# Kernel tuning notes

Measured on AMD Instinct MI355X. Metric: run time of the kernel, lower is better.

The kernel has to match this reference:

```python
import jax, jax.numpy as jnp
import numpy as np

DIM = 512
HEADS = 8
D_HEAD = 64
INNER_FF = 4 * DIM  # 2048
EPS = 1e-5
SCALE = D_HEAD ** -0.5


def _layernorm(x, w, b):
    x = x.astype(jnp.float32)
    mu = jnp.mean(x, axis=-1, keepdims=True)
    var = jnp.mean(jnp.square(x - mu), axis=-1, keepdims=True)
    return (x - mu) * jax.lax.rsqrt(var + EPS) * w + b


def _l2_attn(x, wq, bq, wv, bv, wo, bo):
    # x: [B, N, DIM]. k = q (context is ignored in the original module).
    b, n, _ = x.shape
    q = (x @ wq + bq).reshape(b, n, HEADS, D_HEAD).transpose(0, 2, 1, 3)  # b h n d
    v = (x @ wv + bv).reshape(b, n, HEADS, D_HEAD).transpose(0, 2, 1, 3)
    q = q.astype(jnp.float32)
    AB = jnp.einsum('bhid,bhjd->bhij', q, q)          # [b,h,n,n]
    AA = jnp.sum(jnp.square(q), axis=-1)               # [b,h,n]
    sim = -(AA[..., :, None] - 2.0 * AB + AA[..., None, :]) * SCALE
    attn = jax.nn.softmax(sim, axis=-1)
    out = jnp.einsum('bhij,bhjd->bhid', attn, v)       # [b,h,n,d]
    out = out.transpose(0, 2, 1, 3).reshape(b, n, HEADS * D_HEAD)
    return out @ wo + bo


def _geglu_ff(x, w1, b1, w2, b2):
    h = x @ w1 + b1                      # [B, N, 2*INNER_FF]
    a, gate = jnp.split(h, 2, axis=-1)
    return (a * jax.nn.gelu(gate, approximate=False)) @ w2 + b2


def setup_inputs() -> dict:
    key = jax.random.key(0)
    ks = jax.random.split(key, 24)
    s = 0.02
    d = {'x': jax.random.normal(ks[0], (4, 2048, DIM), jnp.float32)}
    # layernorms
    d['sa_norm_w'] = jnp.ones((DIM,), jnp.float32)
    d['sa_norm_b'] = jnp.zeros((DIM,), jnp.float32)
    d['ca_norm_w'] = jnp.ones((DIM,), jnp.float32)
    d['ca_norm_b'] = jnp.zeros((DIM,), jnp.float32)
    d['ff_norm_w'] = jnp.ones((DIM,), jnp.float32)
    d['ff_norm_b'] = jnp.zeros((DIM,), jnp.float32)
    # attn1 (self)
    d['a1_wq'] = jax.random.normal(ks[1], (DIM, DIM), jnp.float32) * s
    d['a1_bq'] = jnp.zeros((DIM,), jnp.float32)
    d['a1_wv'] = jax.random.normal(ks[2], (DIM, DIM), jnp.float32) * s
    d['a1_bv'] = jnp.zeros((DIM,), jnp.float32)
    d['a1_wo'] = jax.random.normal(ks[3], (DIM, DIM), jnp.float32) * s
    d['a1_bo'] = jnp.zeros((DIM,), jnp.float32)
    # attn2 (cross, but k=q and v from x in original code)
    d['a2_wq'] = jax.random.normal(ks[4], (DIM, DIM), jnp.float32) * s
    d['a2_bq'] = jnp.zeros((DIM,), jnp.float32)
    d['a2_wv'] = jax.random.normal(ks[5], (DIM, DIM), jnp.float32) * s
    d['a2_bv'] = jnp.zeros((DIM,), jnp.float32)
    d['a2_wo'] = jax.random.normal(ks[6], (DIM, DIM), jnp.float32) * s
    d['a2_bo'] = jnp.zeros((DIM,), jnp.float32)
    # GEGLU FFN
    d['ff_w1'] = jax.random.normal(ks[7], (DIM, 2 * INNER_FF), jnp.float32) * s
    d['ff_b1'] = jnp.zeros((2 * INNER_FF,), jnp.float32)
    d['ff_w2'] = jax.random.normal(ks[8], (INNER_FF, DIM), jnp.float32) * s
    d['ff_b2'] = jnp.zeros((DIM,), jnp.float32)
    return d


def reference(x, sa_norm_w, sa_norm_b, ca_norm_w, ca_norm_b, ff_norm_w, ff_norm_b,
              a1_wq, a1_bq, a1_wv, a1_bv, a1_wo, a1_bo,
              a2_wq, a2_bq, a2_wv, a2_bv, a2_wo, a2_bo,
              ff_w1, ff_b1, ff_w2, ff_b2):
    x = _l2_attn(_layernorm(x, sa_norm_w, sa_norm_b), a1_wq, a1_bq, a1_wv, a1_bv, a1_wo, a1_bo) + x
    x = _l2_attn(_layernorm(x, ca_norm_w, ca_norm_b), a2_wq, a2_bq, a2_wv, a2_bv, a2_wo, a2_bo) + x
    x = _geglu_ff(_layernorm(x, ff_norm_w, ff_norm_b), ff_w1, ff_b1, ff_w2, ff_b2) + x
    return x
```

## Files before the change

kernel.cpp:

```cpp
#include <hip/hip_runtime.h>
#include <hip/hip_bf16.h>


typedef short bf16x8 __attribute__((ext_vector_type(8)));
typedef float f32x4 __attribute__((ext_vector_type(4)));
typedef unsigned short u16;
typedef unsigned int u32;

__device__ __forceinline__ float bf2f(u16 u) {
    return __uint_as_float(((u32)u) << 16);
}
__device__ __forceinline__ u16 f2bf(float f) {
    u32 u = __float_as_uint(f);
    u32 rb = ((u >> 16) & 1u) + 0x7fffu;
    return (u16)((u + rb) >> 16);
}
__device__ __forceinline__ float gelu_fast(float x) {
    float y = 1.5957691216f * (x + 0.044715f * x * x * x);
    return x / (1.f + __expf(-y));
}
__device__ __forceinline__ void gl2lds16(const u16* g, u16* l) {
    __builtin_amdgcn_global_load_lds(
        (const __attribute__((address_space(1))) void*)(unsigned long long)(uintptr_t)g,
        (__attribute__((address_space(3))) void*)(unsigned long long)(uintptr_t)l,
        16, 0, 0);
}

struct TArgs {
    const float* src[8];
    u16* dst[8];
    int R[8], C[8];
    int start[9];
};
__global__ __launch_bounds__(256) void transpose_multi(TArgs a) {
    __shared__ float tile[32][33];
    int bid = blockIdx.x;
    int s = 0;
    while (bid >= a.start[s + 1]) s++;
    int local = bid - a.start[s];
    int R = a.R[s], C = a.C[s];
    int tx = C >> 5;
    int bx = local % tx, by = local / tx;
    const float* in = a.src[s];
    u16* out = a.dst[s];
    int t = threadIdx.x;
    int c = t & 31, r0 = (t >> 5) * 4;
#pragma unroll
    for (int i = 0; i < 4; i++)
        tile[r0 + i][c] = in[(size_t)(by * 32 + r0 + i) * C + bx * 32 + c];
    __syncthreads();
#pragma unroll
    for (int i = 0; i < 4; i++)
        out[(size_t)(bx * 32 + r0 + i) * R + by * 32 + c] = f2bf(tile[c][r0 + i]);
}

__global__ __launch_bounds__(256) void ln_kernel(const float* __restrict__ x,
                                                 const float* __restrict__ w,
                                                 const float* __restrict__ b,
                                                 u16* __restrict__ out) {
    int row = blockIdx.x, t = threadIdx.x;
    const float* xr = x + (size_t)row * 512;
    float2 v = *(const float2*)(xr + t * 2);
    float s1 = v.x + v.y;
    float s2 = v.x * v.x + v.y * v.y;
#pragma unroll
    for (int m = 1; m < 64; m <<= 1) {
        s1 += __shfl_xor(s1, m);
        s2 += __shfl_xor(s2, m);
    }
    __shared__ float r1[4], r2[4];
    int wave = t >> 6, lane = t & 63;
    if (lane == 0) { r1[wave] = s1; r2[wave] = s2; }
    __syncthreads();
    float tot1 = r1[0] + r1[1] + r1[2] + r1[3];
    float tot2 = r2[0] + r2[1] + r2[2] + r2[3];
    float mu = tot1 * (1.f / 512.f);
    float var = tot2 * (1.f / 512.f) - mu * mu;
    float rs = rsqrtf(var + 1e-5f);
    float2 wv = *(const float2*)(w + t * 2);
    float2 bv = *(const float2*)(b + t * 2);
    float o0 = (v.x - mu) * rs * wv.x + bv.x;
    float o1 = (v.y - mu) * rs * wv.y + bv.y;
    u32 pack = (u32)f2bf(o0) | ((u32)f2bf(o1) << 16);
    *(u32*)(out + (size_t)row * 512 + t * 2) = pack;
}

__global__ __launch_bounds__(256) void gemm_ff1(const u16* __restrict__ A,
                                                const u16* __restrict__ BT,
                                                const float* __restrict__ bias,
                                                u16* __restrict__ gout,
                                                int K) {
    __shared__ u16 As[2][128 * 32];
    __shared__ u16 Bs[2][128 * 32];
    int t = threadIdx.x;
    int wave = t >> 6, lane = t & 63, quad = lane >> 4, l16 = lane & 15;
    int m0 = blockIdx.x * 128, n0 = blockIdx.y * 64;
    f32x4 aacc[2][4], gacc[2][4];
#pragma unroll
    for (int i = 0; i < 2; i++)
#pragma unroll
        for (int j = 0; j < 4; j++) {
            aacc[i][j] = (f32x4){0.f, 0.f, 0.f, 0.f};
            gacc[i][j] = (f32x4){0.f, 0.f, 0.f, 0.f};
        }
    const u16* Ag = A + (size_t)(m0 + wave * 32 + (lane >> 2)) * K + (lane & 3) * 8;
    int brow = (wave < 2) ? (n0 + wave * 32) : (2048 + n0 + (wave - 2) * 32);
    const u16* Bg = BT + (size_t)(brow + (lane >> 2)) * K + (lane & 3) * 8;
    int lo = wave * 32 * 32;
    const size_t rstep = (size_t)16 * K;
    gl2lds16(Ag, &As[0][lo]);
    gl2lds16(Ag + rstep, &As[0][lo + 16 * 32]);
    gl2lds16(Bg, &Bs[0][lo]);
    gl2lds16(Bg + rstep, &Bs[0][lo + 16 * 32]);
    int buf = 0;
    for (int k0 = 0; k0 < K; k0 += 32, buf ^= 1) {
        int kn = (k0 + 32 < K) ? (k0 + 32) : k0;
        int nb = buf ^ 1;
        asm volatile("s_waitcnt lgkmcnt(0)\n\ts_barrier" ::: "memory");
        gl2lds16(Ag + kn, &As[nb][lo]);
        gl2lds16(Ag + kn + rstep, &As[nb][lo + 16 * 32]);
        gl2lds16(Bg + kn, &Bs[nb][lo]);
        gl2lds16(Bg + kn + rstep, &Bs[nb][lo + 16 * 32]);
        asm volatile("s_waitcnt vmcnt(4)\n\ts_barrier" ::: "memory");
        bf16x8 a[2];
#pragma unroll
        for (int i = 0; i < 2; i++)
            a[i] = *(const bf16x8*)&As[buf][(wave * 32 + i * 16 + l16) * 32 + quad * 8];
#pragma unroll
        for (int j = 0; j < 4; j++) {
            bf16x8 ba = *(const bf16x8*)&Bs[buf][(j * 16 + l16) * 32 + quad * 8];
            bf16x8 bg = *(const bf16x8*)&Bs[buf][(64 + j * 16 + l16) * 32 + quad * 8];
#pragma unroll
            for (int i = 0; i < 2; i++) {
                aacc[i][j] = __builtin_amdgcn_mfma_f32_16x16x32_bf16(a[i], ba, aacc[i][j], 0, 0, 0);
                gacc[i][j] = __builtin_amdgcn_mfma_f32_16x16x32_bf16(a[i], bg, gacc[i][j], 0, 0, 0);
            }
        }
    }
    asm volatile("s_waitcnt vmcnt(0)" ::: "memory");
    int row_base = m0 + wave * 32 + quad * 4;
#pragma unroll
    for (int j = 0; j < 4; j++) {
        int col = n0 + j * 16 + l16;
        float ba = bias[col];
        float bg = bias[2048 + col];
#pragma unroll
        for (int i = 0; i < 2; i++) {
#pragma unroll
            for (int r = 0; r < 4; r++) {
                int row = row_base + i * 16 + r;
                float av = aacc[i][j][r] + ba;
                float gv = gacc[i][j][r] + bg;
                gout[(size_t)row * 2048 + col] = f2bf(av * gelu_fast(gv));
            }
        }
    }
}

template <int MODE>
__global__ __launch_bounds__(256) void gemm_rect(const u16* __restrict__ A,
                                                 const u16* __restrict__ BT,
                                                 const float* __restrict__ bias,
                                                 const float* __restrict__ bias2,
                                                 const float* __restrict__ res,
                                                 float* __restrict__ outf,
                                                 u16* __restrict__ outb,
                                                 u16* __restrict__ outb2,
                                                 float* __restrict__ aa,
                                                 int M, int N, int K) {
    __shared__ u16 As[2][128 * 32];
    __shared__ u16 Bs[2][64 * 32];
    int t = threadIdx.x;
    int wave = t >> 6, lane = t & 63, quad = lane >> 4, l16 = lane & 15;
    int m0 = blockIdx.x * 128, n0 = blockIdx.y * 64;
    f32x4 acc[2][4];
#pragma unroll
    for (int i = 0; i < 2; i++)
#pragma unroll
        for (int j = 0; j < 4; j++) acc[i][j] = (f32x4){0.f, 0.f, 0.f, 0.f};
    const u16* Ag = A + (size_t)(m0 + wave * 32 + (lane >> 2)) * K + (lane & 3) * 8;
    const u16* Bg = BT + (size_t)(n0 + wave * 16 + (lane >> 2)) * K + (lane & 3) * 8;
    int loA = wave * 32 * 32;
    int loB = wave * 16 * 32;
    const size_t rstep = (size_t)16 * K;
    gl2lds16(Ag, &As[0][loA]);
    gl2lds16(Ag + rstep, &As[0][loA + 16 * 32]);
    gl2lds16(Bg, &Bs[0][loB]);
    int buf = 0;
    for (int k0 = 0; k0 < K; k0 += 32, buf ^= 1) {
        int kn = (k0 + 32 < K) ? (k0 + 32) : k0;
        int nb = buf ^ 1;
        asm volatile("s_waitcnt lgkmcnt(0)\n\ts_barrier" ::: "memory");
        gl2lds16(Ag + kn, &As[nb][loA]);
        gl2lds16(Ag + kn + rstep, &As[nb][loA + 16 * 32]);
        gl2lds16(Bg + kn, &Bs[nb][loB]);
        asm volatile("s_waitcnt vmcnt(3)\n\ts_barrier" ::: "memory");
        bf16x8 a[2], b[4];
#pragma unroll
        for (int i = 0; i < 2; i++)
            a[i] = *(const bf16x8*)&As[buf][(wave * 32 + i * 16 + l16) * 32 + quad * 8];
#pragma unroll
        for (int j = 0; j < 4; j++)
            b[j] = *(const bf16x8*)&Bs[buf][(j * 16 + l16) * 32 + quad * 8];
#pragma unroll
        for (int i = 0; i < 2; i++)
#pragma unroll
            for (int j = 0; j < 4; j++)
                acc[i][j] = __builtin_amdgcn_mfma_f32_16x16x32_bf16(a[i], b[j], acc[i][j], 0, 0, 0);
    }
    asm volatile("s_waitcnt vmcnt(0)" ::: "memory");
    int row_base = m0 + wave * 32 + quad * 4;
    float ssq[2][4];
#pragma unroll
    for (int i = 0; i < 2; i++)
#pragma unroll
        for (int r = 0; r < 4; r++) ssq[i][r] = 0.f;
#pragma unroll
    for (int j = 0; j < 4; j++) {
        int col = n0 + j * 16 + l16;
        float bv;
        if (MODE == 4) bv = (col < 512) ? bias[col] : bias2[col - 512];
        else bv = bias[col];
#pragma unroll
        for (int i = 0; i < 2; i++) {
            int rowA = row_base + i * 16;
            if (MODE == 4) {
                if (col < 512) {
                    int hh = col >> 6, d = col & 63;
#pragma unroll
                    for (int r = 0; r < 4; r++) {
                        int row = rowA + r;
                        float v = acc[i][j][r] + bv;
                        ssq[i][r] += v * v;
                        outb[((size_t)((row >> 11) * 8 + hh) * 2048 + (row & 2047)) * 64 + d] = f2bf(v);
                    }
                } else {
                    int c2 = col - 512;
                    int hh = c2 >> 6, d = c2 & 63;
                    int n = rowA & 2047;
                    int a4 = (n >> 2) & 7;
                    int ncol = (n & ~31) + ((a4 & 3) << 3) + ((a4 >> 2) << 2);
                    u32 plo = (u32)f2bf(acc[i][j][0] + bv) | ((u32)f2bf(acc[i][j][1] + bv) << 16);
                    u32 phi = (u32)f2bf(acc[i][j][2] + bv) | ((u32)f2bf(acc[i][j][3] + bv) << 16);
                    uint2 pk; pk.x = plo; pk.y = phi;
                    *(uint2*)&outb2[((size_t)((rowA >> 11) * 8 + hh) * 64 + d) * 2048 + ncol] = pk;
                }
            } else {
#pragma unroll
                for (int r = 0; r < 4; r++) {
                    size_t idx = (size_t)(rowA + r) * N + col;
                    outf[idx] = acc[i][j][r] + bv + res[idx];
                }
            }
        }
    }
    if (MODE == 4 && n0 < 512) {
        int hh = n0 >> 6;
#pragma unroll
        for (int i = 0; i < 2; i++) {
#pragma unroll
            for (int r = 0; r < 4; r++) {
                float s = ssq[i][r];
                s += __shfl_xor(s, 1); s += __shfl_xor(s, 2);
                s += __shfl_xor(s, 4); s += __shfl_xor(s, 8);
                if (l16 == 0) {
                    int row = row_base + i * 16 + r;
                    aa[(size_t)((row >> 11) * 8 + hh) * 2048 + (row & 2047)] = s * 0.125f;
                }
            }
        }
    }
}

__global__ __launch_bounds__(256) void attn_mfma(const u16* __restrict__ qbuf,
                                                 const u16* __restrict__ vtp,
                                                 const float* __restrict__ aas,
                                                 u16* __restrict__ out) {
    __shared__ u16 L[2][8192];
    int bid = blockIdx.x;
    int bh = bid & 31;
    int itile = bid >> 5;
    const u16* qb = qbuf + (size_t)bh * 2048 * 64;
    const u16* vtb = vtp + (size_t)bh * 64 * 2048;
    const float* aab = aas + (size_t)bh * 2048;
    int t = threadIdx.x;
    int wave = t >> 6, lane = t & 63, quad = lane >> 4, l16 = lane & 15;
    int ibase = itile * 128 + wave * 32;
    int sw = l16 & 7;

    bf16x8 qf[2][2];
    float ci[2];
    f32x4 O[2][4];
    float lr[2] = {0.f, 0.f};
#pragma unroll
    for (int st = 0; st < 2; st++) {
        const u16* qr = qb + (size_t)(ibase + st * 16 + l16) * 64;
        qf[st][0] = *(const bf16x8*)(qr + quad * 8);
        qf[st][1] = *(const bf16x8*)(qr + 32 + quad * 8);
        ci[st] = aab[ibase + st * 16 + l16];
#pragma unroll
        for (int nt = 0; nt < 4; nt++) O[st][nt] = (f32x4){0.f, 0.f, 0.f, 0.f};
    }

    int r1 = t >> 3, cs = t & 7;
    int wof1 = r1 * 64 + 8 * (cs ^ (r1 & 7));
    int wof2 = (r1 + 32) * 64 + 8 * (cs ^ (r1 & 7));

    {
        uint4 pq1 = *(const uint4*)(qb + (size_t)r1 * 64 + cs * 8);
        uint4 pq2 = *(const uint4*)(qb + (size_t)(r1 + 32) * 64 + cs * 8);
        uint4 pv1 = *(const uint4*)(vtb + (size_t)r1 * 2048 + cs * 8);
        uint4 pv2 = *(const uint4*)(vtb + (size_t)(r1 + 32) * 2048 + cs * 8);
        *(uint4*)&L[0][wof1] = pq1;
        *(uint4*)&L[0][wof2] = pq2;
        *(uint4*)&L[0][4096 + wof1] = pv1;
        *(uint4*)&L[0][4096 + wof2] = pv2;
    }
    __syncthreads();

    for (int it = 0; it < 32; ++it) {
        int cur = it & 1;
        int j0 = it << 6;
        uint4 pq1, pq2, pv1, pv2;
        bool more = (it + 1 < 32);
        if (more) {
            int j0n = j0 + 64;
            pq1 = *(const uint4*)(qb + (size_t)(j0n + r1) * 64 + cs * 8);
            pq2 = *(const uint4*)(qb + (size_t)(j0n + r1 + 32) * 64 + cs * 8);
            pv1 = *(const uint4*)(vtb + (size_t)r1 * 2048 + j0n + cs * 8);
            pv2 = *(const uint4*)(vtb + (size_t)(r1 + 32) * 2048 + j0n + cs * 8);
        }
        const u16* Q = &L[cur][0];
        const u16* V = &L[cur][4096];
#pragma unroll
        for (int c = 0; c < 2; c++) {
            int r10 = c * 32 + l16, r20 = c * 32 + 16 + l16;
            bf16x8 a10 = *(const bf16x8*)&Q[r10 * 64 + 8 * (quad ^ sw)];
            bf16x8 a11 = *(const bf16x8*)&Q[r10 * 64 + 8 * ((4 + quad) ^ sw)];
            bf16x8 a20 = *(const bf16x8*)&Q[r20 * 64 + 8 * (quad ^ sw)];
            bf16x8 a21 = *(const bf16x8*)&Q[r20 * 64 + 8 * ((4 + quad) ^ sw)];
            f32x4 s0[2], s1[2];
            __builtin_amdgcn_s_setprio(1);
#pragma unroll
            for (int st = 0; st < 2; st++) {
                f32x4 z = {0.f, 0.f, 0.f, 0.f};
                s0[st] = __builtin_amdgcn_mfma_f32_16x16x32_bf16(a10, qf[st][0], z, 0, 0, 0);
                s0[st] = __builtin_amdgcn_mfma_f32_16x16x32_bf16(a11, qf[st][1], s0[st], 0, 0, 0);
                s1[st] = __builtin_amdgcn_mfma_f32_16x16x32_bf16(a20, qf[st][0], z, 0, 0, 0);
                s1[st] = __builtin_amdgcn_mfma_f32_16x16x32_bf16(a21, qf[st][1], s1[st], 0, 0, 0);
            }
            __builtin_amdgcn_s_setprio(0);
            float4 aav0 = *(const float4*)(aab + j0 + c * 32 + quad * 4);
            float4 aav1 = *(const float4*)(aab + j0 + c * 32 + 16 + quad * 4);
            bf16x8 pa[2];
#pragma unroll
            for (int st = 0; st < 2; st++) {
                float p0 = __expf(s0[st][0] * 0.25f - aav0.x - ci[st]);
                float p1 = __expf(s0[st][1] * 0.25f - aav0.y - ci[st]);
                float p2 = __expf(s0[st][2] * 0.25f - aav0.z - ci[st]);
                float p3 = __expf(s0[st][3] * 0.25f - aav0.w - ci[st]);
                float p4 = __expf(s1[st][0] * 0.25f - aav1.x - ci[st]);
                float p5 = __expf(s1[st][1] * 0.25f - aav1.y - ci[st]);
                float p6 = __expf(s1[st][2] * 0.25f - aav1.z - ci[st]);
                float p7 = __expf(s1[st][3] * 0.25f - aav1.w - ci[st]);
                lr[st] += (p0 + p1 + p2 + p3) + (p4 + p5 + p6 + p7);
                u32* pu = (u32*)&pa[st];
                pu[0] = __builtin_amdgcn_perm(__float_as_uint(p1), __float_as_uint(p0), 0x07060302u);
                pu[1] = __builtin_amdgcn_perm(__float_as_uint(p3), __float_as_uint(p2), 0x07060302u);
                pu[2] = __builtin_amdgcn_perm(__float_as_uint(p5), __float_as_uint(p4), 0x07060302u);
                pu[3] = __builtin_amdgcn_perm(__float_as_uint(p7), __float_as_uint(p6), 0x07060302u);
            }
            __builtin_amdgcn_s_setprio(1);
#pragma unroll
            for (int nt = 0; nt < 4; nt++) {
                int rv = nt * 16 + l16;
                bf16x8 vf = *(const bf16x8*)&V[rv * 64 + 8 * ((c * 4 + quad) ^ sw)];
                O[0][nt] = __builtin_amdgcn_mfma_f32_16x16x32_bf16(pa[0], vf, O[0][nt], 0, 0, 0);
                O[1][nt] = __builtin_amdgcn_mfma_f32_16x16x32_bf16(pa[1], vf, O[1][nt], 0, 0, 0);
            }
            __builtin_amdgcn_s_setprio(0);
        }
        if (more) {
            u16* D = &L[cur ^ 1][0];
            *(uint4*)&D[wof1] = pq1;
            *(uint4*)&D[wof2] = pq2;
            *(uint4*)&D[4096 + wof1] = pv1;
            *(uint4*)&D[4096 + wof2] = pv2;
        }
        __syncthreads();
    }

    int b = bh >> 3, h = bh & 7;
#pragma unroll
    for (int st = 0; st < 2; st++) {
        float l = lr[st];
        l += __shfl_xor(l, 16);
        l += __shfl_xor(l, 32);
        float inv = 1.f / l;
#pragma unroll
        for (int r = 0; r < 4; r++) {
            float invr = __shfl(inv, quad * 4 + r);
            size_t row = (size_t)(b * 2048 + ibase + st * 16 + quad * 4 + r);
            u16* o = out + row * 512 + h * 64 + l16;
            o[0]  = f2bf(O[st][0][r] * invr);
            o[16] = f2bf(O[st][1][r] * invr);
            o[32] = f2bf(O[st][2][r] * invr);
            o[48] = f2bf(O[st][3][r] * invr);
        }
    }
}

extern "C" void kernel_launch(void* const* d_in, const int* in_sizes, int n_in,
                              void* d_out, int out_size, void* d_ws, size_t ws_size,
                              hipStream_t stream) {
    const float* x      = (const float*)d_in[0];
    const float* sa_w   = (const float*)d_in[1];
    const float* sa_b   = (const float*)d_in[2];
    const float* ca_w   = (const float*)d_in[3];
    const float* ca_b   = (const float*)d_in[4];
    const float* ffn_w  = (const float*)d_in[5];
    const float* ffn_b  = (const float*)d_in[6];
    const float* a1_wq  = (const float*)d_in[7];
    const float* a1_bq  = (const float*)d_in[8];
    const float* a1_wv  = (const float*)d_in[9];
    const float* a1_bv  = (const float*)d_in[10];
    const float* a1_wo  = (const float*)d_in[11];
    const float* a1_bo  = (const float*)d_in[12];
    const float* a2_wq  = (const float*)d_in[13];
    const float* a2_bq  = (const float*)d_in[14];
    const float* a2_wv  = (const float*)d_in[15];
    const float* a2_bv  = (const float*)d_in[16];
    const float* a2_wo  = (const float*)d_in[17];
    const float* a2_bo  = (const float*)d_in[18];
    const float* ff_w1  = (const float*)d_in[19];
    const float* ff_b1  = (const float*)d_in[20];
    const float* ff_w2  = (const float*)d_in[21];
    const float* ff_b2  = (const float*)d_in[22];

    char* ws = (char*)d_ws;
    const size_t MB = 1ull << 20;
    float* x_res   = (float*)(ws);
    u16* xn        = (u16*)(ws + 16 * MB);
    u16* wT_a1qv   = (u16*)(ws + 24 * MB);
    u16* wT_a2qv   = (u16*)(ws + 25 * MB);
    u16* wT_a1o    = (u16*)(ws + 26 * MB);
    u16* wT_a2o    = (u16*)(ws + 26 * MB + 512 * 1024);
    u16* wT_ff1    = (u16*)(ws + 27 * MB);
    u16* wT_ff2    = (u16*)(ws + 31 * MB);
    u16* qbuf      = (u16*)(ws + 34 * MB);
    u16* vtp       = (u16*)(ws + 42 * MB);
    float* aab     = (float*)(ws + 50 * MB);
    u16* attn_o    = (u16*)(ws + 51 * MB);
    u16* gbuf      = (u16*)(ws + 60 * MB);

    (void)in_sizes; (void)n_in; (void)out_size; (void)ws_size;

    TArgs ta;
    ta.src[0] = a1_wq; ta.dst[0] = wT_a1qv;               ta.R[0] = 512;  ta.C[0] = 512;
    ta.src[1] = a1_wv; ta.dst[1] = wT_a1qv + 512 * 512;   ta.R[1] = 512;  ta.C[1] = 512;
    ta.src[2] = a2_wq; ta.dst[2] = wT_a2qv;               ta.R[2] = 512;  ta.C[2] = 512;
    ta.src[3] = a2_wv; ta.dst[3] = wT_a2qv + 512 * 512;   ta.R[3] = 512;  ta.C[3] = 512;
    ta.src[4] = a1_wo; ta.dst[4] = wT_a1o;                ta.R[4] = 512;  ta.C[4] = 512;
    ta.src[5] = a2_wo; ta.dst[5] = wT_a2o;                ta.R[5] = 512;  ta.C[5] = 512;
    ta.src[6] = ff_w1; ta.dst[6] = wT_ff1;                ta.R[6] = 512;  ta.C[6] = 4096;
    ta.src[7] = ff_w2; ta.dst[7] = wT_ff2;                ta.R[7] = 2048; ta.C[7] = 512;
    ta.start[0] = 0;
    for (int s = 0; s < 8; s++)
        ta.start[s + 1] = ta.start[s] + (ta.C[s] >> 5) * (ta.R[s] >> 5);
    transpose_multi<<<ta.start[8], 256, 0, stream>>>(ta);

    ln_kernel<<<8192, 256, 0, stream>>>(x, sa_w, sa_b, xn);
    gemm_rect<4><<<dim3(64, 16), 256, 0, stream>>>(xn, wT_a1qv, a1_bq, a1_bv, nullptr, nullptr, qbuf, vtp, aab, 8192, 1024, 512);
    attn_mfma<<<512, 256, 0, stream>>>(qbuf, vtp, aab, attn_o);
    gemm_rect<2><<<dim3(64, 8), 256, 0, stream>>>(attn_o, wT_a1o, a1_bo, nullptr, x, x_res, nullptr, nullptr, nullptr, 8192, 512, 512);

    ln_kernel<<<8192, 256, 0, stream>>>(x_res, ca_w, ca_b, xn);
    gemm_rect<4><<<dim3(64, 16), 256, 0, stream>>>(xn, wT_a2qv, a2_bq, a2_bv, nullptr, nullptr, qbuf, vtp, aab, 8192, 1024, 512);
    attn_mfma<<<512, 256, 0, stream>>>(qbuf, vtp, aab, attn_o);
    gemm_rect<2><<<dim3(64, 8), 256, 0, stream>>>(attn_o, wT_a2o, a2_bo, nullptr, x_res, x_res, nullptr, nullptr, nullptr, 8192, 512, 512);

    ln_kernel<<<8192, 256, 0, stream>>>(x_res, ffn_w, ffn_b, xn);
    gemm_ff1<<<dim3(64, 32), 256, 0, stream>>>(xn, wT_ff1, ff_b1, gbuf, 512);
    gemm_rect<2><<<dim3(64, 8), 256, 0, stream>>>(gbuf, wT_ff2, ff_b2, nullptr, x_res, (float*)d_out, nullptr, nullptr, nullptr, 8192, 512, 2048);
}
```

Measured before the change: 384.9 us.

## Double attention key tile to 128 and use exp2 with folded scale

Processes 128 keys per loop iteration instead of 64, doubling the LDS double buffer and reorganising the V tile layout with a wider swizzle, which halves the number of loop iterations and block barriers. The softmax exponent is rewritten as exp2 of an FMA with the log2e factor folded into the precomputed squared-norm term, and the per-query norm term is dropped since it cancels in normalisation. This cuts ALU work per score but removes the stabilising shift, risking overflow for large norms, and the larger LDS footprint may reduce occupancy.

Measured after the change: 399.4 us. 1.04x slower.

```diff
diff --git a/kernel.cpp b/kernel.cpp
--- a/kernel.cpp
+++ b/kernel.cpp
@@ -265,7 +265,7 @@
                 s += __shfl_xor(s, 4); s += __shfl_xor(s, 8);
                 if (l16 == 0) {
                     int row = row_base + i * 16 + r;
-                    aa[(size_t)((row >> 11) * 8 + hh) * 2048 + (row & 2047)] = s * 0.125f;
+                    aa[(size_t)((row >> 11) * 8 + hh) * 2048 + (row & 2047)] = s * 0.18033688f;
                 }
             }
         }
@@ -276,7 +276,7 @@
                                                  const u16* __restrict__ vtp,
                                                  const float* __restrict__ aas,
                                                  u16* __restrict__ out) {
-    __shared__ u16 L[2][8192];
+    __shared__ u16 L[2][16384];
     int bid = blockIdx.x;
     int bh = bid & 31;
     int itile = bid >> 5;
@@ -285,11 +285,10 @@
     const float* aab = aas + (size_t)bh * 2048;
     int t = threadIdx.x;
     int wave = t >> 6, lane = t & 63, quad = lane >> 4, l16 = lane & 15;
+    int sw7 = l16 & 7;
     int ibase = itile * 128 + wave * 32;
-    int sw = l16 & 7;
 
     bf16x8 qf[2][2];
-    float ci[2];
     f32x4 O[2][4];
     float lr[2] = {0.f, 0.f};
 #pragma unroll
@@ -297,48 +296,49 @@
         const u16* qr = qb + (size_t)(ibase + st * 16 + l16) * 64;
         qf[st][0] = *(const bf16x8*)(qr + quad * 8);
         qf[st][1] = *(const bf16x8*)(qr + 32 + quad * 8);
-        ci[st] = aab[ibase + st * 16 + l16];
 #pragma unroll
         for (int nt = 0; nt < 4; nt++) O[st][nt] = (f32x4){0.f, 0.f, 0.f, 0.f};
     }
 
-    int r1 = t >> 3, cs = t & 7;
-    int wof1 = r1 * 64 + 8 * (cs ^ (r1 & 7));
-    int wof2 = (r1 + 32) * 64 + 8 * (cs ^ (r1 & 7));
-
-    {
-        uint4 pq1 = *(const uint4*)(qb + (size_t)r1 * 64 + cs * 8);
-        uint4 pq2 = *(const uint4*)(qb + (size_t)(r1 + 32) * 64 + cs * 8);
-        uint4 pv1 = *(const uint4*)(vtb + (size_t)r1 * 2048 + cs * 8);
-        uint4 pv2 = *(const uint4*)(vtb + (size_t)(r1 + 32) * 2048 + cs * 8);
-        *(uint4*)&L[0][wof1] = pq1;
-        *(uint4*)&L[0][wof2] = pq2;
-        *(uint4*)&L[0][4096 + wof1] = pv1;
-        *(uint4*)&L[0][4096 + wof2] = pv2;
+    int qrow[4], qcs[4], qwof[4], vrow[4], vsl[4], vwof[4];
+#pragma unroll
+    for (int k = 0; k < 4; k++) {
+        int s = t + k * 256;
+        qrow[k] = s >> 3; qcs[k] = s & 7;
+        qwof[k] = qrow[k] * 64 + 8 * (qcs[k] ^ (qrow[k] & 7));
+        vrow[k] = s >> 4; vsl[k] = s & 15;
+        vwof[k] = 8192 + vrow[k] * 128 + 8 * ((vsl[k] & 8) | ((vsl[k] & 7) ^ (vrow[k] & 7)));
+    }
+#pragma unroll
+    for (int k = 0; k < 4; k++) {
+        *(uint4*)&L[0][qwof[k]] = *(const uint4*)(qb + (size_t)qrow[k] * 64 + qcs[k] * 8);
+        *(uint4*)&L[0][vwof[k]] = *(const uint4*)(vtb + (size_t)vrow[k] * 2048 + vsl[k] * 8);
     }
     __syncthreads();
 
-    for (int it = 0; it < 32; ++it) {
+    const float C0 = 0.36067376f;
+    for (int it = 0; it < 16; ++it) {
         int cur = it & 1;
-        int j0 = it << 6;
-        uint4 pq1, pq2, pv1, pv2;
-        bool more = (it + 1 < 32);
+        int j0 = it << 7;
+        uint4 pq[4], pv[4];
+        bool more = (it + 1 < 16);
         if (more) {
-            int j0n = j0 + 64;
-            pq1 = *(const uint4*)(qb + (size_t)(j0n + r1) * 64 + cs * 8);
-            pq2 = *(const uint4*)(qb + (size_t)(j0n + r1 + 32) * 64 + cs * 8);
-            pv1 = *(const uint4*)(vtb + (size_t)r1 * 2048 + j0n + cs * 8);
-            pv2 = *(const uint4*)(vtb + (size_t)(r1 + 32) * 2048 + j0n + cs * 8);
+            int j0n = j0 + 128;
+#pragma unroll
+            for (int k = 0; k < 4; k++) {
+                pq[k] = *(const uint4*)(qb + (size_t)(j0n + qrow[k]) * 64 + qcs[k] * 8);
+                pv[k] = *(const uint4*)(vtb + (size_t)vrow[k] * 2048 + j0n + vsl[k] * 8);
+            }
         }
         const u16* Q = &L[cur][0];
-        const u16* V = &L[cur][4096];
-#pragma unroll
-        for (int c = 0; c < 2; c++) {
+        const u16* V = &L[cur][8192];
+#pragma unroll
+        for (int c = 0; c < 4; c++) {
             int r10 = c * 32 + l16, r20 = c * 32 + 16 + l16;
-            bf16x8 a10 = *(const bf16x8*)&Q[r10 * 64 + 8 * (quad ^ sw)];
-            bf16x8 a11 = *(const bf16x8*)&Q[r10 * 64 + 8 * ((4 + quad) ^ sw)];
-            bf16x8 a20 = *(const bf16x8*)&Q[r20 * 64 + 8 * (quad ^ sw)];
-            bf16x8 a21 = *(const bf16x8*)&Q[r20 * 64 + 8 * ((4 + quad) ^ sw)];
+            bf16x8 a10 = *(const bf16x8*)&Q[r10 * 64 + 8 * (quad ^ sw7)];
+            bf16x8 a11 = *(const bf16x8*)&Q[r10 * 64 + 8 * ((4 + quad) ^ sw7)];
+            bf16x8 a20 = *(const bf16x8*)&Q[r20 * 64 + 8 * (quad ^ sw7)];
+            bf16x8 a21 = *(const bf16x8*)&Q[r20 * 64 + 8 * ((4 + quad) ^ sw7)];
             f32x4 s0[2], s1[2];
             __builtin_amdgcn_s_setprio(1);
 #pragma unroll
@@ -355,14 +355,14 @@
             bf16x8 pa[2];
 #pragma unroll
             for (int st = 0; st < 2; st++) {
-                float p0 = __expf(s0[st][0] * 0.25f - aav0.x - ci[st]);
-                float p1 = __expf(s0[st][1] * 0.25f - aav0.y - ci[st]);
-                float p2 = __expf(s0[st][2] * 0.25f - aav0.z - ci[st]);
-                float p3 = __expf(s0[st][3] * 0.25f - aav0.w - ci[st]);
-                float p4 = __expf(s1[st][0] * 0.25f - aav1.x - ci[st]);
-                float p5 = __expf(s1[st][1] * 0.25f - aav1.y - ci[st]);
-                float p6 = __expf(s1[st][2] * 0.25f - aav1.z - ci[st]);
-                float p7 = __expf(s1[st][3] * 0.25f - aav1.w - ci[st]);
+                float p0 = __builtin_amdgcn_exp2f(fmaf(s0[st][0], C0, -aav0.x));
+                float p1 = __builtin_amdgcn_exp2f(fmaf(s0[st][1], C0, -aav0.y));
+                float p2 = __builtin_amdgcn_exp2f(fmaf(s0[st][2], C0, -aav0.z));
+                float p3 = __builtin_amdgcn_exp2f(fmaf(s0[st][3], C0, -aav0.w));
+                float p4 = __builtin_amdgcn_exp2f(fmaf(s1[st][0], C0, -aav1.x));
+                float p5 = __builtin_amdgcn_exp2f(fmaf(s1[st][1], C0, -aav1.y));
+                float p6 = __builtin_amdgcn_exp2f(fmaf(s1[st][2], C0, -aav1.z));
+                float p7 = __builtin_amdgcn_exp2f(fmaf(s1[st][3], C0, -aav1.w));
                 lr[st] += (p0 + p1 + p2 + p3) + (p4 + p5 + p6 + p7);
                 u32* pu = (u32*)&pa[st];
                 pu[0] = __builtin_amdgcn_perm(__float_as_uint(p1), __float_as_uint(p0), 0x07060302u);
@@ -373,8 +373,8 @@
             __builtin_amdgcn_s_setprio(1);
 #pragma unroll
             for (int nt = 0; nt < 4; nt++) {
-                int rv = nt * 16 + l16;
-                bf16x8 vf = *(const bf16x8*)&V[rv * 64 + 8 * ((c * 4 + quad) ^ sw)];
+                int sl = c * 4 + quad;
+                bf16x8 vf = *(const bf16x8*)&V[(nt * 16 + l16) * 128 + 8 * ((sl & 8) | ((sl & 7) ^ sw7))];
                 O[0][nt] = __builtin_amdgcn_mfma_f32_16x16x32_bf16(pa[0], vf, O[0][nt], 0, 0, 0);
                 O[1][nt] = __builtin_amdgcn_mfma_f32_16x16x32_bf16(pa[1], vf, O[1][nt], 0, 0, 0);
             }
@@ -382,10 +382,11 @@
         }
         if (more) {
             u16* D = &L[cur ^ 1][0];
-            *(uint4*)&D[wof1] = pq1;
-            *(uint4*)&D[wof2] = pq2;
-            *(uint4*)&D[4096 + wof1] = pv1;
-            *(uint4*)&D[4096 + wof2] = pv2;
+#pragma unroll
+            for (int k = 0; k < 4; k++) {
+                *(uint4*)&D[qwof[k]] = pq[k];
+                *(uint4*)&D[vwof[k]] = pv[k];
+            }
         }
         __syncthreads();
     }
```
